# Kernel optimization log

Hardware: AMD Instinct MI355X
Metric: run time of the kernel (lower is better)

Reference implementation:

```python
import jax, jax.numpy as jnp
import numpy as np

FMF_A, FMF_B, FMF_C, FMF_D = 0.0, 0.3, 0.7, 1.0

def fmf(x):
    # max(min((x-a)/(b-a), (d-x)/(d-c)), 0)
    rise = (x - FMF_A) / (FMF_B - FMF_A)
    fall = (FMF_D - x) / (FMF_D - FMF_C)
    return jnp.maximum(jnp.minimum(rise, fall), 0.0)

def setup_inputs() -> dict:
    key = jax.random.key(0)
    ks = jax.random.split(key, 7)
    B, S, D = 4, 4096, 512
    H = D // 2
    s = 0.02
    return {
        "x": jax.random.normal(ks[0], (B, S, D), dtype=jnp.float32),
        "Wq": jax.random.normal(ks[1], (D, H), dtype=jnp.float32) * s,
        "bq": jnp.zeros((H,), dtype=jnp.float32),
        "Wk": jax.random.normal(ks[2], (D, H), dtype=jnp.float32) * s,
        "bk": jnp.zeros((H,), dtype=jnp.float32),
        "Wv": jax.random.normal(ks[3], (D, D), dtype=jnp.float32) * s,
        "bv": jnp.zeros((D,), dtype=jnp.float32),
    }

def reference(x, Wq, bq, Wk, bk, Wv, bv):
    H = Wq.shape[1]
    q = x @ Wq + bq                      # [B,S,H]
    k = x @ Wk + bk                      # [B,S,H]
    v = x @ Wv + bv                      # [B,S,D]
    scores = jnp.einsum('bqh,bkh->bqk', q, k) / jnp.sqrt(jnp.float32(H))
    attn = jax.nn.softmax(scores, axis=-1)   # [B,S,S]
    attn = fmf(attn)                         # fuzzy clamp, breaks row-stochasticity
    out = jnp.einsum('bqk,bkd->bqd', attn, v)
    return out, attn
```

## Files before the change

kernel.cpp:

```cpp
#include <hip/hip_runtime.h>
#include <hip/hip_bf16.h>

typedef __attribute__((ext_vector_type(8))) short bf16x8;
typedef __attribute__((ext_vector_type(4))) float f32x4;
typedef __attribute__((ext_vector_type(16))) float f32x16;

#define MFMA16(a, b, c) __builtin_amdgcn_mfma_f32_16x16x32_bf16(a, b, c, 0, 0, 0)
#define MFMA32(a, b, c) __builtin_amdgcn_mfma_f32_32x32x16_bf16(a, b, c, 0, 0, 0)

static constexpr int S  = 4096;
static constexpr int Dm = 512;
static constexpr int Hh = 256;
static constexpr int Bb = 4;

__device__ __forceinline__ int idx256(int r, int c) { return r * 256 + (c ^ ((r & 7) << 3)); }
__device__ __forceinline__ int idx64 (int r, int c) { return r * 64  + (c ^ ((r & 7) << 3)); }

__global__ __launch_bounds__(256) void proj_kernel(
    const float* __restrict__ X,
    const float* __restrict__ W,
    const float* __restrict__ bias,
    __hip_bfloat16* __restrict__ out,
    int N, float scale, int transpose_out)
{
    __shared__ __hip_bfloat16 a_lds[2][64][32];
    __shared__ __hip_bfloat16 w_lds[2][64][32];

    const int tid  = threadIdx.x;
    const int lane = tid & 63;
    const int wave = tid >> 6;
    const int lr   = lane & 15;
    const int lg   = lane >> 4;
    const int m0   = blockIdx.y * 64;
    const int n0   = blockIdx.x * 64;

    const int arow = tid >> 2, aoff = (tid & 3) * 8;
    const int wkk  = tid >> 3, wnoff = (tid & 7) * 8;
    const float* asrc = X + (size_t)(m0 + arow) * 512 + aoff;
    const float* wsrc = W + (size_t)wkk * N + n0 + wnoff;

    f32x4 acc[4];
    #pragma unroll
    for (int n = 0; n < 4; ++n) acc[n] = (f32x4){0.f, 0.f, 0.f, 0.f};

    {
        float ar[8], wr[8];
        #pragma unroll
        for (int j = 0; j < 8; ++j) { ar[j] = asrc[j]; wr[j] = wsrc[j]; }
        #pragma unroll
        for (int j = 0; j < 8; ++j) a_lds[0][arow][aoff + j] = __float2bfloat16(ar[j]);
        #pragma unroll
        for (int j = 0; j < 8; ++j) w_lds[0][wnoff + j][wkk] = __float2bfloat16(wr[j]);
    }
    __syncthreads();

    int cur = 0;
    for (int k0 = 0; k0 < 512; k0 += 32) {
        float ar[8], wr[8];
        if (k0 < 480) {
            #pragma unroll
            for (int j = 0; j < 8; ++j) ar[j] = asrc[k0 + 32 + j];
            #pragma unroll
            for (int j = 0; j < 8; ++j) wr[j] = wsrc[(size_t)(k0 + 32) * N + j];
        }
        bf16x8 af = *(const bf16x8*)&a_lds[cur][wave * 16 + lr][lg * 8];
        __builtin_amdgcn_s_setprio(1);
        #pragma unroll
        for (int n = 0; n < 4; ++n) {
            bf16x8 bfr = *(const bf16x8*)&w_lds[cur][n * 16 + lr][lg * 8];
            acc[n] = MFMA16(af, bfr, acc[n]);
        }
        __builtin_amdgcn_s_setprio(0);
        if (k0 < 480) {
            #pragma unroll
            for (int j = 0; j < 8; ++j) a_lds[cur ^ 1][arow][aoff + j] = __float2bfloat16(ar[j]);
            #pragma unroll
            for (int j = 0; j < 8; ++j) w_lds[cur ^ 1][wnoff + j][wkk] = __float2bfloat16(wr[j]);
        }
        __syncthreads();
        cur ^= 1;
    }

    #pragma unroll
    for (int n = 0; n < 4; ++n) {
        int col = n0 + n * 16 + lr;
        float bia = bias[col];
        #pragma unroll
        for (int r = 0; r < 4; ++r) {
            int row = m0 + wave * 16 + lg * 4 + r;
            float val = (acc[n][r] + bia) * scale;
            if (!transpose_out) {
                out[(size_t)row * N + col] = __float2bfloat16(val);
            } else {
                int bidx = row >> 12, s = row & 4095;
                out[((size_t)bidx * N + col) * S + s] = __float2bfloat16(val);
            }
        }
    }
}

__global__ __launch_bounds__(512, 4) void lsum_kernel(
    const __hip_bfloat16* __restrict__ Q,
    const __hip_bfloat16* __restrict__ K,
    float* __restrict__ l_ws)
{
    __shared__ __hip_bfloat16 k_lds[64 * 256];
    __shared__ float stats_lds[2][128];

    const int bx      = blockIdx.x;
    const int logical = (bx & 7) * 64 + (bx >> 3);
    const int b       = logical >> 7;
    const int kvq     = (logical >> 5) & 3;
    const int q0      = (logical & 31) * 128;

    const int tid  = threadIdx.x;
    const int lane = tid & 63;
    const int w    = tid >> 6;
    const int l31  = lane & 31;
    const int hi   = lane >> 5;
    const int qg   = w >> 1;
    const int cg   = w & 1;

    const __hip_bfloat16* Qb = Q + ((size_t)b * S + q0) * Hh;
    const __hip_bfloat16* Kb = K + (size_t)b * S * Hh;

    bf16x8 qf[16];
    #pragma unroll
    for (int t = 0; t < 16; ++t)
        qf[t] = *(const bf16x8*)&Qb[(size_t)(qg * 32 + l31) * Hh + t * 16 + hi * 8];

    float lsum[16];
    #pragma unroll
    for (int j = 0; j < 16; ++j) lsum[j] = 0.f;

    const int krow = tid >> 3, kcb = (tid & 7) * 8;

    for (int kt = kvq * 16; kt < kvq * 16 + 16; ++kt) {
        __syncthreads();
        {
            const __hip_bfloat16* src = Kb + (size_t)(kt * 64 + krow) * Hh + kcb;
            #pragma unroll
            for (int c0 = 0; c0 < 4; ++c0)
                *(uint4*)&k_lds[idx256(krow, kcb + c0 * 64)] = *(const uint4*)&src[c0 * 64];
        }
        __syncthreads();

        f32x16 acc;
        #pragma unroll
        for (int j = 0; j < 16; ++j) acc[j] = 0.f;
        __builtin_amdgcn_s_setprio(1);
        #pragma unroll
        for (int t = 0; t < 16; ++t) {
            bf16x8 kf = *(const bf16x8*)&k_lds[idx256(cg * 32 + l31, t * 16 + hi * 8)];
            acc = MFMA32(qf[t], kf, acc);
        }
        __builtin_amdgcn_s_setprio(0);
        #pragma unroll
        for (int j = 0; j < 16; ++j) lsum[j] += __expf(acc[j]);
    }

    #pragma unroll
    for (int j = 0; j < 16; ++j)
        #pragma unroll
        for (int m = 1; m < 32; m <<= 1) lsum[j] += __shfl_xor(lsum[j], m);

    if (l31 == 0) {
        #pragma unroll
        for (int j = 0; j < 16; ++j) {
            int row = qg * 32 + (j & 3) + 8 * (j >> 2) + 4 * hi;
            stats_lds[cg][row] = lsum[j];
        }
    }
    __syncthreads();
    if (tid < 128) {
        l_ws[((size_t)(b * S + q0 + tid)) * 4 + kvq] =
            stats_lds[0][tid] + stats_lds[1][tid];
    }
}

__global__ __launch_bounds__(512, 4) void pv_kernel(
    const __hip_bfloat16* __restrict__ Q,
    const __hip_bfloat16* __restrict__ K,
    const __hip_bfloat16* __restrict__ VT,
    const float* __restrict__ l_ws,
    float* __restrict__ out,
    float* __restrict__ attn)
{
    __shared__ __align__(16) char smem[73728];
    __hip_bfloat16* k_lds  = (__hip_bfloat16*)smem;
    __hip_bfloat16* vt_lds = (__hip_bfloat16*)(smem + 32768);
    __hip_bfloat16* p_lds  = (__hip_bfloat16*)(smem + 65536);

    const int bx      = blockIdx.x;
    const int logical = (bx & 7) * 64 + (bx >> 3);
    const int b       = logical >> 7;
    const int dh      = (logical >> 6) & 1;
    const int q0      = (logical & 63) * 64;

    const int tid  = threadIdx.x;
    const int lane = tid & 63;
    const int w    = tid >> 6;
    const int lr   = lane & 15;
    const int lg   = lane >> 4;
    const int qg   = w >> 1;
    const int half = w & 1;

    const __hip_bfloat16* Qb  = Q  + ((size_t)b * S + q0) * Hh;
    const __hip_bfloat16* Kb  = K  + (size_t)b * S * Hh;
    const __hip_bfloat16* VTb = VT + ((size_t)b * Dm + dh * 256) * S;

    bf16x8 qf[8];
    #pragma unroll
    for (int h = 0; h < 8; ++h)
        qf[h] = *(const bf16x8*)&Qb[(size_t)(qg * 16 + lr) * Hh + h * 32 + lg * 8];

    float inv_l[4];
    #pragma unroll
    for (int r = 0; r < 4; ++r) {
        int row = q0 + qg * 16 + lg * 4 + r;
        float4 lp = *(const float4*)&l_ws[((size_t)(b * S + row)) * 4];
        inv_l[r] = 1.0f / (lp.x + lp.y + lp.z + lp.w);
    }

    const int krow = tid >> 3, kcb = (tid & 7) * 8;
    const int vrow = tid >> 3, vcb = (tid & 7) * 8;

    f32x4 oacc[4][2];
    #pragma unroll
    for (int qt = 0; qt < 4; ++qt)
        #pragma unroll
        for (int dt = 0; dt < 2; ++dt) oacc[qt][dt] = (f32x4){0.f, 0.f, 0.f, 0.f};

    for (int kt = 0; kt < 64; ++kt) {
        __syncthreads();
        {
            const __hip_bfloat16* src = Kb + (size_t)(kt * 64 + krow) * Hh + kcb;
            #pragma unroll
            for (int c0 = 0; c0 < 4; ++c0)
                *(uint4*)&k_lds[idx256(krow, kcb + c0 * 64)] = *(const uint4*)&src[c0 * 64];
        }
        __syncthreads();

        f32x4 acc[2];
        #pragma unroll
        for (int nn = 0; nn < 2; ++nn) acc[nn] = (f32x4){0.f, 0.f, 0.f, 0.f};
        __builtin_amdgcn_s_setprio(1);
        #pragma unroll
        for (int nn = 0; nn < 2; ++nn) {
            int n = half * 2 + nn;
            #pragma unroll
            for (int h = 0; h < 8; ++h) {
                bf16x8 kf = *(const bf16x8*)&k_lds[idx256(n * 16 + lr, h * 32 + lg * 8)];
                acc[nn] = MFMA16(qf[h], kf, acc[nn]);
            }
        }
        __builtin_amdgcn_s_setprio(0);

        {
            #pragma unroll
            for (int j = 0; j < 4; ++j) {
                int row = j * 64 + vrow;
                *(uint4*)&vt_lds[idx64(row, vcb)] =
                    *(const uint4*)&VTb[(size_t)row * S + kt * 64 + vcb];
            }
        }

        #pragma unroll
        for (int nn = 0; nn < 2; ++nn)
            #pragma unroll
            for (int r = 0; r < 4; ++r) {
                float p = __expf(acc[nn][r]) * inv_l[r];
                float f = fmaxf(fminf(p, 1.0f - p) * (1.0f / 0.3f), 0.0f);
                int row_l = qg * 16 + lg * 4 + r;
                int col_l = (half * 2 + nn) * 16 + lr;
                if (dh == 0)
                    attn[((size_t)(b * S + q0 + row_l)) * S + kt * 64 + col_l] = f;
                p_lds[idx64(row_l, col_l)] = __float2bfloat16(f);
            }
        __syncthreads();

        bf16x8 pf[4][2];
        #pragma unroll
        for (int qt = 0; qt < 4; ++qt)
            #pragma unroll
            for (int ks = 0; ks < 2; ++ks)
                pf[qt][ks] = *(const bf16x8*)&p_lds[idx64(qt * 16 + lr, ks * 32 + lg * 8)];
        __builtin_amdgcn_s_setprio(1);
        #pragma unroll
        for (int dt = 0; dt < 2; ++dt)
            #pragma unroll
            for (int ks = 0; ks < 2; ++ks) {
                bf16x8 vf = *(const bf16x8*)&vt_lds[idx64(w * 32 + dt * 16 + lr, ks * 32 + lg * 8)];
                #pragma unroll
                for (int qt = 0; qt < 4; ++qt)
                    oacc[qt][dt] = MFMA16(pf[qt][ks], vf, oacc[qt][dt]);
            }
        __builtin_amdgcn_s_setprio(0);
    }

    #pragma unroll
    for (int qt = 0; qt < 4; ++qt)
        #pragma unroll
        for (int dt = 0; dt < 2; ++dt) {
            int col = dh * 256 + w * 32 + dt * 16 + lr;
            #pragma unroll
            for (int r = 0; r < 4; ++r) {
                int row = q0 + qt * 16 + lg * 4 + r;
                out[((size_t)(b * S + row)) * Dm + col] = oacc[qt][dt][r];
            }
        }
}

extern "C" void kernel_launch(void* const* d_in, const int* in_sizes, int n_in,
                              void* d_out, int out_size, void* d_ws, size_t ws_size,
                              hipStream_t stream) {
    const float* x  = (const float*)d_in[0];
    const float* Wq = (const float*)d_in[1];
    const float* bq = (const float*)d_in[2];
    const float* Wk = (const float*)d_in[3];
    const float* bk = (const float*)d_in[4];
    const float* Wv = (const float*)d_in[5];
    const float* bv = (const float*)d_in[6];

    float* out  = (float*)d_out;
    float* attn = out + (size_t)Bb * S * Dm;

    __hip_bfloat16* q_ws  = (__hip_bfloat16*)d_ws;
    __hip_bfloat16* k_ws  = q_ws + (size_t)Bb * S * Hh;
    __hip_bfloat16* vt_ws = k_ws + (size_t)Bb * S * Hh;
    float*          l_ws  = (float*)(vt_ws + (size_t)Bb * Dm * S);

    const float scale = 0.0625f;

    proj_kernel<<<dim3(Hh / 64, (Bb * S) / 64), 256, 0, stream>>>(x, Wq, bq, q_ws, Hh, scale, 0);
    proj_kernel<<<dim3(Hh / 64, (Bb * S) / 64), 256, 0, stream>>>(x, Wk, bk, k_ws, Hh, 1.0f, 0);
    proj_kernel<<<dim3(Dm / 64, (Bb * S) / 64), 256, 0, stream>>>(x, Wv, bv, vt_ws, Dm, 1.0f, 1);

    lsum_kernel<<<512, 512, 0, stream>>>(q_ws, k_ws, l_ws);
    pv_kernel<<<512, 512, 0, stream>>>(q_ws, k_ws, vt_ws, l_ws, out, attn);
}
```

Measured before the change: 497.2 us.

## Double-buffer K tiles with register prefetch and load V fragments directly

Both the row-sum kernel and the PV kernel now double-buffer the K tile in LDS. Each iteration prefetches the next K tile into registers while computing on the current one, then stores it to the other buffer, so only one barrier per iteration is needed instead of two. In the PV kernel the V^T LDS staging is removed: each wave loads its own V fragments straight from global memory into registers, which frees that LDS space for the second K buffer. The cost is more register pressure and strided, less coalesced global reads of V, which rely on cache hits.

New measurement: 914.7 us. +84.0%, slower.

```diff
diff --git a/kernel.cpp b/kernel.cpp
--- a/kernel.cpp
+++ b/kernel.cpp
@@ -104,7 +104,7 @@
     const __hip_bfloat16* __restrict__ K,
     float* __restrict__ l_ws)
 {
-    __shared__ __hip_bfloat16 k_lds[64 * 256];
+    __shared__ __hip_bfloat16 k_lds[2][64 * 256];
     __shared__ float stats_lds[2][128];
 
     const int bx      = blockIdx.x;
@@ -134,16 +134,27 @@
     for (int j = 0; j < 16; ++j) lsum[j] = 0.f;
 
     const int krow = tid >> 3, kcb = (tid & 7) * 8;
-
-    for (int kt = kvq * 16; kt < kvq * 16 + 16; ++kt) {
-        __syncthreads();
-        {
-            const __hip_bfloat16* src = Kb + (size_t)(kt * 64 + krow) * Hh + kcb;
-            #pragma unroll
-            for (int c0 = 0; c0 < 4; ++c0)
-                *(uint4*)&k_lds[idx256(krow, kcb + c0 * 64)] = *(const uint4*)&src[c0 * 64];
-        }
-        __syncthreads();
+    const int kt0  = kvq * 16;
+
+    {
+        uint4 kr[4];
+        const __hip_bfloat16* src = Kb + (size_t)(kt0 * 64 + krow) * Hh + kcb;
+        #pragma unroll
+        for (int c0 = 0; c0 < 4; ++c0) kr[c0] = *(const uint4*)&src[c0 * 64];
+        #pragma unroll
+        for (int c0 = 0; c0 < 4; ++c0)
+            *(uint4*)&k_lds[0][idx256(krow, kcb + c0 * 64)] = kr[c0];
+    }
+    __syncthreads();
+
+    int cur = 0;
+    for (int kt = 0; kt < 16; ++kt) {
+        uint4 kr[4];
+        if (kt < 15) {
+            const __hip_bfloat16* src = Kb + (size_t)((kt0 + kt + 1) * 64 + krow) * Hh + kcb;
+            #pragma unroll
+            for (int c0 = 0; c0 < 4; ++c0) kr[c0] = *(const uint4*)&src[c0 * 64];
+        }
 
         f32x16 acc;
         #pragma unroll
@@ -151,12 +162,20 @@
         __builtin_amdgcn_s_setprio(1);
         #pragma unroll
         for (int t = 0; t < 16; ++t) {
-            bf16x8 kf = *(const bf16x8*)&k_lds[idx256(cg * 32 + l31, t * 16 + hi * 8)];
+            bf16x8 kf = *(const bf16x8*)&k_lds[cur][idx256(cg * 32 + l31, t * 16 + hi * 8)];
             acc = MFMA32(qf[t], kf, acc);
         }
         __builtin_amdgcn_s_setprio(0);
         #pragma unroll
         for (int j = 0; j < 16; ++j) lsum[j] += __expf(acc[j]);
+
+        if (kt < 15) {
+            #pragma unroll
+            for (int c0 = 0; c0 < 4; ++c0)
+                *(uint4*)&k_lds[cur ^ 1][idx256(krow, kcb + c0 * 64)] = kr[c0];
+        }
+        __syncthreads();
+        cur ^= 1;
     }
 
     #pragma unroll
@@ -187,8 +206,8 @@
     float* __restrict__ attn)
 {
     __shared__ __align__(16) char smem[73728];
-    __hip_bfloat16* k_lds  = (__hip_bfloat16*)smem;
-    __hip_bfloat16* vt_lds = (__hip_bfloat16*)(smem + 32768);
+    __hip_bfloat16* k_lds0 = (__hip_bfloat16*)smem;
+    __hip_bfloat16* k_lds1 = (__hip_bfloat16*)(smem + 32768);
     __hip_bfloat16* p_lds  = (__hip_bfloat16*)(smem + 65536);
 
     const int bx      = blockIdx.x;
@@ -223,7 +242,8 @@
     }
 
     const int krow = tid >> 3, kcb = (tid & 7) * 8;
-    const int vrow = tid >> 3, vcb = (tid & 7) * 8;
+    const __hip_bfloat16* vrow0 = VTb + (size_t)(w * 32 + lr) * S;
+    const __hip_bfloat16* vrow1 = VTb + (size_t)(w * 32 + 16 + lr) * S;
 
     f32x4 oacc[4][2];
     #pragma unroll
@@ -231,15 +251,34 @@
         #pragma unroll
         for (int dt = 0; dt < 2; ++dt) oacc[qt][dt] = (f32x4){0.f, 0.f, 0.f, 0.f};
 
+    {
+        uint4 kr[4];
+        const __hip_bfloat16* src = Kb + (size_t)krow * Hh + kcb;
+        #pragma unroll
+        for (int c0 = 0; c0 < 4; ++c0) kr[c0] = *(const uint4*)&src[c0 * 64];
+        #pragma unroll
+        for (int c0 = 0; c0 < 4; ++c0)
+            *(uint4*)&k_lds0[idx256(krow, kcb + c0 * 64)] = kr[c0];
+    }
+    __syncthreads();
+
+    int cur = 0;
     for (int kt = 0; kt < 64; ++kt) {
-        __syncthreads();
-        {
-            const __hip_bfloat16* src = Kb + (size_t)(kt * 64 + krow) * Hh + kcb;
-            #pragma unroll
-            for (int c0 = 0; c0 < 4; ++c0)
-                *(uint4*)&k_lds[idx256(krow, kcb + c0 * 64)] = *(const uint4*)&src[c0 * 64];
-        }
-        __syncthreads();
+        __hip_bfloat16* kbuf_cur = cur ? k_lds1 : k_lds0;
+        __hip_bfloat16* kbuf_nxt = cur ? k_lds0 : k_lds1;
+
+        uint4 kr[4];
+        if (kt < 63) {
+            const __hip_bfloat16* src = Kb + (size_t)((kt + 1) * 64 + krow) * Hh + kcb;
+            #pragma unroll
+            for (int c0 = 0; c0 < 4; ++c0) kr[c0] = *(const uint4*)&src[c0 * 64];
+        }
+        bf16x8 vf[2][2];
+        #pragma unroll
+        for (int ks = 0; ks < 2; ++ks) {
+            vf[0][ks] = *(const bf16x8*)&vrow0[kt * 64 + ks * 32 + lg * 8];
+            vf[1][ks] = *(const bf16x8*)&vrow1[kt * 64 + ks * 32 + lg * 8];
+        }
 
         f32x4 acc[2];
         #pragma unroll
@@ -250,20 +289,11 @@
             int n = half * 2 + nn;
             #pragma unroll
             for (int h = 0; h < 8; ++h) {
-                bf16x8 kf = *(const bf16x8*)&k_lds[idx256(n * 16 + lr, h * 32 + lg * 8)];
+                bf16x8 kf = *(const bf16x8*)&kbuf_cur[idx256(n * 16 + lr, h * 32 + lg * 8)];
                 acc[nn] = MFMA16(qf[h], kf, acc[nn]);
             }
         }
         __builtin_amdgcn_s_setprio(0);
-
-        {
-            #pragma unroll
-            for (int j = 0; j < 4; ++j) {
-                int row = j * 64 + vrow;
-                *(uint4*)&vt_lds[idx64(row, vcb)] =
-                    *(const uint4*)&VTb[(size_t)row * S + kt * 64 + vcb];
-            }
-        }
 
         #pragma unroll
         for (int nn = 0; nn < 2; ++nn)
@@ -289,13 +319,19 @@
         #pragma unroll
         for (int dt = 0; dt < 2; ++dt)
             #pragma unroll
-            for (int ks = 0; ks < 2; ++ks) {
-                bf16x8 vf = *(const bf16x8*)&vt_lds[idx64(w * 32 + dt * 16 + lr, ks * 32 + lg * 8)];
+            for (int ks = 0; ks < 2; ++ks)
                 #pragma unroll
                 for (int qt = 0; qt < 4; ++qt)
-                    oacc[qt][dt] = MFMA16(pf[qt][ks], vf, oacc[qt][dt]);
-            }
+                    oacc[qt][dt] = MFMA16(pf[qt][ks], vf[dt][ks], oacc[qt][dt]);
         __builtin_amdgcn_s_setprio(0);
+
+        if (kt < 63) {
+            #pragma unroll
+            for (int c0 = 0; c0 < 4; ++c0)
+                *(uint4*)&kbuf_nxt[idx256(krow, kcb + c0 * 64)] = kr[c0];
+        }
+        __syncthreads();
+        cur ^= 1;
     }
 
     #pragma unroll
```
